# Performance work log

Hardware: AMD Instinct MI355X
Metric: run time of the kernel (lower is better)

The kernel has to match this reference:

```python
import jax, jax.numpy as jnp
import numpy as np
from functools import partial

DIM = 128      # LSTM hidden size
NODES = 81     # graph nodes
T = 12         # sequence length


def _lstm_layer(x, Wih, Whh, bih, bhh):
    """PyTorch-style LSTM layer. x: (N, T, in) -> (N, T, H). Gate order i,f,g,o."""
    N = x.shape[0]
    H = Whh.shape[1]
    b = bih + bhh

    def step(carry, xt):
        h, c = carry
        gates = xt @ Wih.T + h @ Whh.T + b              # (N, 4H)
        i, f, g, o = jnp.split(gates, 4, axis=-1)
        i = jax.nn.sigmoid(i)
        f = jax.nn.sigmoid(f)
        g = jnp.tanh(g)
        o = jax.nn.sigmoid(o)
        c = f * c + i * g
        h = o * jnp.tanh(c)
        return (h, c), h

    h0 = jnp.zeros((N, H), x.dtype)
    c0 = jnp.zeros((N, H), x.dtype)
    xT = jnp.swapaxes(x, 0, 1)                           # (T, N, in)
    _, hs = jax.lax.scan(step, (h0, c0), xT)
    return jnp.swapaxes(hs, 0, 1)                        # (N, T, H)


def setup_inputs() -> dict:
    key = jax.random.key(0)
    ks = jax.random.split(key, 16)
    k = 1.0 / np.sqrt(DIM)
    u = lambda kk, shape: jax.random.uniform(kk, shape, jnp.float32, -k, k)
    inp = {
        "g_data": jax.random.normal(ks[0], (512, T, NODES), jnp.float32),
        "weights": jax.random.normal(ks[1], (NODES, NODES), jnp.float32) * 0.1,
        # LSTM layer 0 (input size 1)
        "Wih0": u(ks[2], (4 * DIM, 1)),
        "Whh0": u(ks[3], (4 * DIM, DIM)),
        "bih0": u(ks[4], (4 * DIM,)),
        "bhh0": u(ks[5], (4 * DIM,)),
        # LSTM layer 1 (input size DIM)
        "Wih1": u(ks[6], (4 * DIM, DIM)),
        "Whh1": u(ks[7], (4 * DIM, DIM)),
        "bih1": u(ks[8], (4 * DIM,)),
        "bhh1": u(ks[9], (4 * DIM,)),
        # MLP head 128 -> 32 -> 1
        "fc1_w": u(ks[10], (32, DIM)),
        "fc1_b": u(ks[11], (32,)),
        "fc2_w": u(ks[12], (1, 32)),
        "fc2_b": u(ks[13], (1,)),
    }
    return inp


def reference(g_data, weights, Wih0, Whh0, bih0, bhh0, Wih1, Whh1, bih1, bhh1,
              fc1_w, fc1_b, fc2_w, fc2_b):
    B = g_data.shape[0]
    # Vectorized graph aggregation: income[:, :, i] = g_data @ weights[:, i]
    income = jnp.einsum('bta,an->bnt', g_data, weights)   # (B, 81, 12)
    x = income.reshape(B * NODES, T, 1)                   # one scalar seq per (sample, node)
    h1 = _lstm_layer(x, Wih0, Whh0, bih0, bhh0)           # (B*81, 12, 128)
    h2 = _lstm_layer(h1, Wih1, Whh1, bih1, bhh1)          # (B*81, 12, 128)
    last = h2[:, -1, :]                                   # only last step feeds the output
    hid = jax.nn.relu(last @ fc1_w.T + fc1_b)             # (B*81, 32)
    out = jax.nn.relu(hid @ fc2_w.T + fc2_b)              # (B*81, 1)
    return out.reshape(B, NODES).reshape(B, 1, NODES, 1)
```

## Files before the change

kernel.cpp:

```cpp
#include <hip/hip_runtime.h>
#include <math.h>

#define NODES 81
#define T_STEPS 12
#define NSEQ 41472
#define HID 128
#define SEQB 32

typedef unsigned short ushort;
typedef unsigned int uint;
typedef __attribute__((ext_vector_type(8))) _Float16 half8;
typedef __attribute__((ext_vector_type(4))) float f32x4;

#define MFMA(A, B, C) __builtin_amdgcn_mfma_f32_16x16x32_f16((A), (B), (C), 0, 0, 0)

__device__ __forceinline__ float sigf(float v) {
    return __builtin_amdgcn_rcpf(1.f + __builtin_amdgcn_exp2f(v * -1.442695041f));
}
__device__ __forceinline__ float tanhf_(float v) {
    return fmaf(2.f, __builtin_amdgcn_rcpf(1.f + __builtin_amdgcn_exp2f(v * -2.885390082f)), -1.f);
}

__global__ void prep_kernel(const float* __restrict__ Whh0,
                            const float* __restrict__ Wih1,
                            const float* __restrict__ Whh1,
                            const float* __restrict__ Wih0,
                            const float* __restrict__ bih0, const float* __restrict__ bhh0,
                            const float* __restrict__ bih1, const float* __restrict__ bhh1,
                            _Float16* __restrict__ WF0,
                            _Float16* __restrict__ WF1i,
                            _Float16* __restrict__ WF1h,
                            float* __restrict__ wq,
                            float* __restrict__ b0q,
                            float* __restrict__ b1q)
{
    int idx = blockIdx.x * 256 + threadIdx.x;
    if (idx < 196608) {
        int mat = idx >> 16;
        int li  = idx & 65535;
        int j   = li & 7;
        int l   = (li >> 3) & 63;
        int nt  = (li >> 9) & 31;
        int ks  = li >> 14;
        int k = ks * 32 + (l >> 4) * 8 + j;
        int n = nt * 16 + (l & 15);
        const float* W = (mat == 0) ? Whh0 : (mat == 1 ? Wih1 : Whh1);
        _Float16* D = (mat == 0) ? WF0 : (mat == 1 ? WF1i : WF1h);
        D[li] = (_Float16)W[n * 128 + k];
    } else if (idx < 197120) {
        int jp = idx - 196608;
        int u = jp >> 2, t4 = jp & 3;
        wq[jp] = Wih0[t4 * 128 + u];
    } else if (idx < 197632) {
        int jp = idx - 197120;
        int u = jp >> 2, t4 = jp & 3;
        b0q[jp] = bih0[t4 * 128 + u] + bhh0[t4 * 128 + u];
    } else if (idx < 198144) {
        int jp = idx - 197632;
        int u = jp >> 2, t4 = jp & 3;
        b1q[jp] = bih1[t4 * 128 + u] + bhh1[t4 * 128 + u];
    }
}

__global__ void income_kernel(const float* __restrict__ g_data,
                              const float* __restrict__ w,
                              float* __restrict__ x)
{
    int idx = blockIdx.x * 256 + threadIdx.x;
    int n = idx % NODES;
    int r = idx / NODES;
    int t = r % T_STEPS;
    int b = r / T_STEPS;
    const float* grow = g_data + (b * T_STEPS + t) * NODES;
    float s = 0.f;
    #pragma unroll 3
    for (int a = 0; a < NODES; ++a)
        s += grow[a] * w[a * NODES + n];
    x[t * NSEQ + b * NODES + n] = s;
}

__global__ __launch_bounds__(512, 1) void lstm_main(
    const float* __restrict__ x,
    const _Float16* __restrict__ WF0,
    const _Float16* __restrict__ WF1i,
    const _Float16* __restrict__ WF1h,
    const float* __restrict__ wq,
    const float* __restrict__ b0q,
    const float* __restrict__ b1q,
    const float* __restrict__ fc1_w,
    const float* __restrict__ fc1_b,
    const float* __restrict__ fc2_w,
    const float* __restrict__ fc2_b,
    float* __restrict__ out)
{
    __shared__ __align__(16) _Float16 hA0[8192];
    __shared__ __align__(16) _Float16 hA1[8192];

    const int tid = threadIdx.x;
    const int l   = tid & 63;
    const int gr  = tid >> 6;
    const int l15 = l & 15;
    const int l16 = l >> 4;
    const int u   = gr * 16 + l15;
    const int seq0 = blockIdx.x * SEQB;

    for (int i = tid; i < 4096; i += 512) {
        ((uint*)hA0)[i] = 0u; ((uint*)hA1)[i] = 0u;
    }

    const _Float16* wfb0 = WF0  + gr * 512 + l * 8;
    const _Float16* wfb1 = WF1i + gr * 512 + l * 8;
    const _Float16* wfb2 = WF1h + gr * 512 + l * 8;
    half8 B0[4][4], B1[4][4], B2[4][4];
    #pragma unroll
    for (int ks = 0; ks < 4; ++ks)
        #pragma unroll
        for (int t4 = 0; t4 < 4; ++t4) {
            B0[ks][t4] = *(const half8*)(wfb0 + ks * 16384 + t4 * 4096);
            B1[ks][t4] = *(const half8*)(wfb1 + ks * 16384 + t4 * 4096);
            B2[ks][t4] = *(const half8*)(wfb2 + ks * 16384 + t4 * 4096);
        }

    const float4 wv  = *(const float4*)(wq  + u * 4);
    const float4 bv0 = *(const float4*)(b0q + u * 4);
    const float4 bv1 = *(const float4*)(b1q + u * 4);

    float c0[8], c1[8];
    #pragma unroll
    for (int i = 0; i < 8; ++i) { c0[i] = 0.f; c1[i] = 0.f; }
    __syncthreads();

    const int wrbase = (u >> 3) * 256 + (u & 7);

    int cur = 0;
    for (int t = 0; t < T_STEPS; ++t) {
        const int nxt = cur ^ 1;
        const float4 xv0 = *(const float4*)(x + t * NSEQ + seq0 + l16 * 4);
        const float4 xv1 = *(const float4*)(x + t * NSEQ + seq0 + 16 + l16 * 4);

        f32x4 acc[2][4];

        #pragma unroll
        for (int mt = 0; mt < 2; ++mt)
            #pragma unroll
            for (int t4 = 0; t4 < 4; ++t4) acc[mt][t4] = (f32x4){0.f, 0.f, 0.f, 0.f};
        #pragma unroll
        for (int ks = 0; ks < 4; ++ks) {
            const int ao = cur * 4096 + (ks * 4 + l16) * 256 + l15 * 8;
            half8 a0 = *(const half8*)(hA0 + ao);
            half8 a1 = *(const half8*)(hA0 + ao + 128);
            #pragma unroll
            for (int t4 = 0; t4 < 4; ++t4) {
                acc[0][t4] = MFMA(a0, B0[ks][t4], acc[0][t4]);
                acc[1][t4] = MFMA(a1, B0[ks][t4], acc[1][t4]);
            }
        }
        #pragma unroll
        for (int mt = 0; mt < 2; ++mt) {
            #pragma unroll
            for (int r = 0; r < 4; ++r) {
                int m = mt * 16 + l16 * 4 + r;
                float xvr = mt ? xv1[r] : xv0[r];
                float gi = acc[mt][0][r] + xvr * wv.x + bv0.x;
                float gf = acc[mt][1][r] + xvr * wv.y + bv0.y;
                float gg = acc[mt][2][r] + xvr * wv.z + bv0.z;
                float go = acc[mt][3][r] + xvr * wv.w + bv0.w;
                float iv = sigf(gi), fv = sigf(gf), gv = tanhf_(gg), ov = sigf(go);
                float c = fv * c0[mt * 4 + r] + iv * gv;
                c0[mt * 4 + r] = c;
                hA0[nxt * 4096 + wrbase + m * 8] = (_Float16)(ov * tanhf_(c));
            }
        }
        __syncthreads();

        #pragma unroll
        for (int mt = 0; mt < 2; ++mt)
            #pragma unroll
            for (int t4 = 0; t4 < 4; ++t4) acc[mt][t4] = (f32x4){0.f, 0.f, 0.f, 0.f};
        #pragma unroll
        for (int ks = 0; ks < 4; ++ks) {
            const int ao = nxt * 4096 + (ks * 4 + l16) * 256 + l15 * 8;
            half8 a0 = *(const half8*)(hA0 + ao);
            half8 a1 = *(const half8*)(hA0 + ao + 128);
            #pragma unroll
            for (int t4 = 0; t4 < 4; ++t4) {
                acc[0][t4] = MFMA(a0, B1[ks][t4], acc[0][t4]);
                acc[1][t4] = MFMA(a1, B1[ks][t4], acc[1][t4]);
            }
        }
        #pragma unroll
        for (int ks = 0; ks < 4; ++ks) {
            const int ao = cur * 4096 + (ks * 4 + l16) * 256 + l15 * 8;
            half8 a0 = *(const half8*)(hA1 + ao);
            half8 a1 = *(const half8*)(hA1 + ao + 128);
            #pragma unroll
            for (int t4 = 0; t4 < 4; ++t4) {
                acc[0][t4] = MFMA(a0, B2[ks][t4], acc[0][t4]);
                acc[1][t4] = MFMA(a1, B2[ks][t4], acc[1][t4]);
            }
        }
        #pragma unroll
        for (int mt = 0; mt < 2; ++mt) {
            #pragma unroll
            for (int r = 0; r < 4; ++r) {
                int m = mt * 16 + l16 * 4 + r;
                float gi = acc[mt][0][r] + bv1.x;
                float gf = acc[mt][1][r] + bv1.y;
                float gg = acc[mt][2][r] + bv1.z;
                float go = acc[mt][3][r] + bv1.w;
                float iv = sigf(gi), fv = sigf(gf), gv = tanhf_(gg), ov = sigf(go);
                float c = fv * c1[mt * 4 + r] + iv * gv;
                c1[mt * 4 + r] = c;
                hA1[nxt * 4096 + wrbase + m * 8] = (_Float16)(ov * tanhf_(c));
            }
        }
        cur = nxt;
    }
    __syncthreads();

    float* hidb = (float*)hA0;
    float hv[2];
    #pragma unroll
    for (int r2 = 0; r2 < 2; ++r2) {
        int task = tid + r2 * 512;
        int s = task >> 5, j = task & 31;
        float sum = fc1_b[j];
        const float* wrow = fc1_w + j * HID;
        #pragma unroll 4
        for (int kq = 0; kq < 16; ++kq) {
            half8 H = *(const half8*)(hA1 + cur * 4096 + kq * 256 + s * 8);
            #pragma unroll
            for (int j8 = 0; j8 < 8; ++j8)
                sum += (float)H[j8] * wrow[kq * 8 + j8];
        }
        hv[r2] = fmaxf(sum, 0.f);
    }
    __syncthreads();
    #pragma unroll
    for (int r2 = 0; r2 < 2; ++r2) {
        int task = tid + r2 * 512;
        hidb[(task >> 5) * 33 + (task & 31)] = hv[r2];
    }
    __syncthreads();
    if (tid < SEQB) {
        float sum = fc2_b[0];
        #pragma unroll
        for (int j = 0; j < 32; ++j) sum += hidb[tid * 33 + j] * fc2_w[j];
        out[seq0 + tid] = fmaxf(sum, 0.f);
    }
}

extern "C" void kernel_launch(void* const* d_in, const int* in_sizes, int n_in,
                              void* d_out, int out_size, void* d_ws, size_t ws_size,
                              hipStream_t stream)
{
    const float* g_data = (const float*)d_in[0];
    const float* weights = (const float*)d_in[1];
    const float* Wih0   = (const float*)d_in[2];
    const float* Whh0   = (const float*)d_in[3];
    const float* bih0   = (const float*)d_in[4];
    const float* bhh0   = (const float*)d_in[5];
    const float* Wih1   = (const float*)d_in[6];
    const float* Whh1   = (const float*)d_in[7];
    const float* bih1   = (const float*)d_in[8];
    const float* bhh1   = (const float*)d_in[9];
    const float* fc1_w  = (const float*)d_in[10];
    const float* fc1_b  = (const float*)d_in[11];
    const float* fc2_w  = (const float*)d_in[12];
    const float* fc2_b  = (const float*)d_in[13];
    float* out = (float*)d_out;

    float* ws = (float*)d_ws;
    float*     x    = ws;
    _Float16*  WF0  = (_Float16*)(x + NSEQ * T_STEPS);
    _Float16*  WF1i = WF0 + 65536;
    _Float16*  WF1h = WF1i + 65536;
    float*     wqp  = (float*)(WF1h + 65536);
    float*     b0q  = wqp + 512;
    float*     b1q  = b0q + 512;

    prep_kernel<<<774, 256, 0, stream>>>(Whh0, Wih1, Whh1, Wih0, bih0, bhh0, bih1, bhh1,
                                         WF0, WF1i, WF1h, wqp, b0q, b1q);
    income_kernel<<<1944, 256, 0, stream>>>(g_data, weights, x);
    lstm_main<<<NSEQ / SEQB, 512, 0, stream>>>(x, WF0, WF1i, WF1h, wqp, b0q, b1q,
                                               fc1_w, fc1_b, fc2_w, fc2_b, out);
}
```

Before: 439.9 us.

## Stream LSTM weight fragments from global per step instead of holding them in registers

The kernel no longer preloads all three recurrent and input weight matrices into 48 half8 registers per lane. Each timestep now loads the B fragments from global memory (likely L2/L1 resident), and the gate accumulation is split into two halves separated by a sched_barrier so fewer accumulators are live at once. This is meant to cut VGPR pressure and raise occupancy, or to avoid spills. The cost is repeated global weight loads and twice the LDS A-fragment reads on every step of the recurrence.

```diff
diff --git a/kernel.cpp b/kernel.cpp
--- a/kernel.cpp
+++ b/kernel.cpp
@@ -111,15 +111,6 @@
     const _Float16* wfb0 = WF0  + gr * 512 + l * 8;
     const _Float16* wfb1 = WF1i + gr * 512 + l * 8;
     const _Float16* wfb2 = WF1h + gr * 512 + l * 8;
-    half8 B0[4][4], B1[4][4], B2[4][4];
-    #pragma unroll
-    for (int ks = 0; ks < 4; ++ks)
-        #pragma unroll
-        for (int t4 = 0; t4 < 4; ++t4) {
-            B0[ks][t4] = *(const half8*)(wfb0 + ks * 16384 + t4 * 4096);
-            B1[ks][t4] = *(const half8*)(wfb1 + ks * 16384 + t4 * 4096);
-            B2[ks][t4] = *(const half8*)(wfb2 + ks * 16384 + t4 * 4096);
-        }
 
     const float4 wv  = *(const float4*)(wq  + u * 4);
     const float4 bv0 = *(const float4*)(b0q + u * 4);
@@ -138,22 +129,43 @@
         const float4 xv0 = *(const float4*)(x + t * NSEQ + seq0 + l16 * 4);
         const float4 xv1 = *(const float4*)(x + t * NSEQ + seq0 + 16 + l16 * 4);
 
-        f32x4 acc[2][4];
+        f32x4 acc[2][2];
+        f32x4 sg[2][2];
 
         #pragma unroll
         for (int mt = 0; mt < 2; ++mt)
             #pragma unroll
-            for (int t4 = 0; t4 < 4; ++t4) acc[mt][t4] = (f32x4){0.f, 0.f, 0.f, 0.f};
+            for (int th = 0; th < 2; ++th) acc[mt][th] = (f32x4){0.f, 0.f, 0.f, 0.f};
         #pragma unroll
         for (int ks = 0; ks < 4; ++ks) {
             const int ao = cur * 4096 + (ks * 4 + l16) * 256 + l15 * 8;
             half8 a0 = *(const half8*)(hA0 + ao);
             half8 a1 = *(const half8*)(hA0 + ao + 128);
-            #pragma unroll
-            for (int t4 = 0; t4 < 4; ++t4) {
-                acc[0][t4] = MFMA(a0, B0[ks][t4], acc[0][t4]);
-                acc[1][t4] = MFMA(a1, B0[ks][t4], acc[1][t4]);
-            }
+            half8 b0 = *(const half8*)(wfb0 + ks * 16384 + 0 * 4096);
+            half8 b1 = *(const half8*)(wfb0 + ks * 16384 + 1 * 4096);
+            acc[0][0] = MFMA(a0, b0, acc[0][0]);
+            acc[1][0] = MFMA(a1, b0, acc[1][0]);
+            acc[0][1] = MFMA(a0, b1, acc[0][1]);
+            acc[1][1] = MFMA(a1, b1, acc[1][1]);
+        }
+        sg[0][0] = acc[0][0]; sg[0][1] = acc[0][1];
+        sg[1][0] = acc[1][0]; sg[1][1] = acc[1][1];
+        __builtin_amdgcn_sched_barrier(0);
+        #pragma unroll
+        for (int mt = 0; mt < 2; ++mt)
+            #pragma unroll
+            for (int th = 0; th < 2; ++th) acc[mt][th] = (f32x4){0.f, 0.f, 0.f, 0.f};
+        #pragma unroll
+        for (int ks = 0; ks < 4; ++ks) {
+            const int ao = cur * 4096 + (ks * 4 + l16) * 256 + l15 * 8;
+            half8 a0 = *(const half8*)(hA0 + ao);
+            half8 a1 = *(const half8*)(hA0 + ao + 128);
+            half8 b2 = *(const half8*)(wfb0 + ks * 16384 + 2 * 4096);
+            half8 b3 = *(const half8*)(wfb0 + ks * 16384 + 3 * 4096);
+            acc[0][0] = MFMA(a0, b2, acc[0][0]);
+            acc[1][0] = MFMA(a1, b2, acc[1][0]);
+            acc[0][1] = MFMA(a0, b3, acc[0][1]);
+            acc[1][1] = MFMA(a1, b3, acc[1][1]);
         }
         #pragma unroll
         for (int mt = 0; mt < 2; ++mt) {
@@ -161,10 +173,10 @@
             for (int r = 0; r < 4; ++r) {
                 int m = mt * 16 + l16 * 4 + r;
                 float xvr = mt ? xv1[r] : xv0[r];
-                float gi = acc[mt][0][r] + xvr * wv.x + bv0.x;
-                float gf = acc[mt][1][r] + xvr * wv.y + bv0.y;
-                float gg = acc[mt][2][r] + xvr * wv.z + bv0.z;
-                float go = acc[mt][3][r] + xvr * wv.w + bv0.w;
+                float gi = sg[mt][0][r]  + xvr * wv.x + bv0.x;
+                float gf = sg[mt][1][r]  + xvr * wv.y + bv0.y;
+                float gg = acc[mt][0][r] + xvr * wv.z + bv0.z;
+                float go = acc[mt][1][r] + xvr * wv.w + bv0.w;
                 float iv = sigf(gi), fv = sigf(gf), gv = tanhf_(gg), ov = sigf(go);
                 float c = fv * c0[mt * 4 + r] + iv * gv;
                 c0[mt * 4 + r] = c;
@@ -176,38 +188,71 @@
         #pragma unroll
         for (int mt = 0; mt < 2; ++mt)
             #pragma unroll
-            for (int t4 = 0; t4 < 4; ++t4) acc[mt][t4] = (f32x4){0.f, 0.f, 0.f, 0.f};
+            for (int th = 0; th < 2; ++th) acc[mt][th] = (f32x4){0.f, 0.f, 0.f, 0.f};
         #pragma unroll
         for (int ks = 0; ks < 4; ++ks) {
             const int ao = nxt * 4096 + (ks * 4 + l16) * 256 + l15 * 8;
             half8 a0 = *(const half8*)(hA0 + ao);
             half8 a1 = *(const half8*)(hA0 + ao + 128);
-            #pragma unroll
-            for (int t4 = 0; t4 < 4; ++t4) {
-                acc[0][t4] = MFMA(a0, B1[ks][t4], acc[0][t4]);
-                acc[1][t4] = MFMA(a1, B1[ks][t4], acc[1][t4]);
-            }
+            half8 b0 = *(const half8*)(wfb1 + ks * 16384 + 0 * 4096);
+            half8 b1 = *(const half8*)(wfb1 + ks * 16384 + 1 * 4096);
+            acc[0][0] = MFMA(a0, b0, acc[0][0]);
+            acc[1][0] = MFMA(a1, b0, acc[1][0]);
+            acc[0][1] = MFMA(a0, b1, acc[0][1]);
+            acc[1][1] = MFMA(a1, b1, acc[1][1]);
         }
         #pragma unroll
         for (int ks = 0; ks < 4; ++ks) {
             const int ao = cur * 4096 + (ks * 4 + l16) * 256 + l15 * 8;
             half8 a0 = *(const half8*)(hA1 + ao);
             half8 a1 = *(const half8*)(hA1 + ao + 128);
-            #pragma unroll
-            for (int t4 = 0; t4 < 4; ++t4) {
-                acc[0][t4] = MFMA(a0, B2[ks][t4], acc[0][t4]);
-                acc[1][t4] = MFMA(a1, B2[ks][t4], acc[1][t4]);
-            }
+            half8 b0 = *(const half8*)(wfb2 + ks * 16384 + 0 * 4096);
+            half8 b1 = *(const half8*)(wfb2 + ks * 16384 + 1 * 4096);
+            acc[0][0] = MFMA(a0, b0, acc[0][0]);
+            acc[1][0] = MFMA(a1, b0, acc[1][0]);
+            acc[0][1] = MFMA(a0, b1, acc[0][1]);
+            acc[1][1] = MFMA(a1, b1, acc[1][1]);
+        }
+        sg[0][0] = acc[0][0]; sg[0][1] = acc[0][1];
+        sg[1][0] = acc[1][0]; sg[1][1] = acc[1][1];
+        __builtin_amdgcn_sched_barrier(0);
+        #pragma unroll
+        for (int mt = 0; mt < 2; ++mt)
+            #pragma unroll
+            for (int th = 0; th < 2; ++th) acc[mt][th] = (f32x4){0.f, 0.f, 0.f, 0.f};
+        #pragma unroll
+        for (int ks = 0; ks < 4; ++ks) {
+            const int ao = nxt * 4096 + (ks * 4 + l16) * 256 + l15 * 8;
+            half8 a0 = *(const half8*)(hA0 + ao);
+            half8 a1 = *(const half8*)(hA0 + ao + 128);
+            half8 b2 = *(const half8*)(wfb1 + ks * 16384 + 2 * 4096);
+            half8 b3 = *(const half8*)(wfb1 + ks * 16384 + 3 * 4096);
+            acc[0][0] = MFMA(a0, b2, acc[0][0]);
+            acc[1][0] = MFMA(a1, b2, acc[1][0]);
+            acc[0][1] = MFMA(a0, b3, acc[0][1]);
+            acc[1][1] = MFMA(a1, b3, acc[1][1]);
+        }
+        #pragma unroll
+        for (int ks = 0; ks < 4; ++ks) {
+            const int ao = cur * 4096 + (ks * 4 + l16) * 256 + l15 * 8;
+            half8 a0 = *(const half8*)(hA1 + ao);
+            half8 a1 = *(const half8*)(hA1 + ao + 128);
+            half8 b2 = *(const half8*)(wfb2 + ks * 16384 + 2 * 4096);
+            half8 b3 = *(const half8*)(wfb2 + ks * 16384 + 3 * 4096);
+            acc[0][0] = MFMA(a0, b2, acc[0][0]);
+            acc[1][0] = MFMA(a1, b2, acc[1][0]);
+            acc[0][1] = MFMA(a0, b3, acc[0][1]);
+            acc[1][1] = MFMA(a1, b3, acc[1][1]);
         }
         #pragma unroll
         for (int mt = 0; mt < 2; ++mt) {
             #pragma unroll
             for (int r = 0; r < 4; ++r) {
                 int m = mt * 16 + l16 * 4 + r;
-                float gi = acc[mt][0][r] + bv1.x;
-                float gf = acc[mt][1][r] + bv1.y;
-                float gg = acc[mt][2][r] + bv1.z;
-                float go = acc[mt][3][r] + bv1.w;
+                float gi = sg[mt][0][r]  + bv1.x;
+                float gf = sg[mt][1][r]  + bv1.y;
+                float gg = acc[mt][0][r] + bv1.z;
+                float go = acc[mt][1][r] + bv1.w;
                 float iv = sigf(gi), fv = sigf(gf), gv = tanhf_(gg), ov = sigf(go);
                 float c = fv * c1[mt * 4 + r] + iv * gv;
                 c1[mt * 4 + r] = c;
```

After: 486.2 us. 10.5% more time.
